# Kernel optimization log

Measured on AMD Instinct MI355X. Metric: run time of the kernel, lower is better.

## Reference

```python
import jax, jax.numpy as jnp
import numpy as np

INF = 1e5
EPS = 1e-8
B, NRES, NRIG = 1, 448, 512
C_S, C_Z, C_H, H, PQ, PV = 384, 128, 16, 12, 4, 8


def _quat_to_rot(q):
    q = q / jnp.linalg.norm(q, axis=-1, keepdims=True)
    w, x, y, z = q[..., 0], q[..., 1], q[..., 2], q[..., 3]
    return jnp.stack([
        jnp.stack([1 - 2 * (y * y + z * z), 2 * (x * y - w * z), 2 * (x * z + w * y)], -1),
        jnp.stack([2 * (x * y + w * z), 1 - 2 * (x * x + z * z), 2 * (y * z - w * x)], -1),
        jnp.stack([2 * (x * z - w * y), 2 * (y * z + w * x), 1 - 2 * (x * x + y * y)], -1),
    ], -2)


def setup_inputs() -> dict:
    key = jax.random.key(0)
    ks = jax.random.split(key, 16)
    lin = lambda k, i, o: (jax.random.normal(k, (i, o), jnp.float32) / np.sqrt(i))
    hc = H * C_H
    return dict(
        s=jax.random.normal(ks[0], (B, NRIG, C_S), jnp.float32),
        z=jax.random.normal(ks[1], (B, NRES, NRES, C_Z), jnp.float32),
        rot=_quat_to_rot(jax.random.normal(ks[2], (B, NRIG, 4), jnp.float32)),
        trans=jax.random.normal(ks[3], (B, NRIG, 3), jnp.float32) * 10.0,
        mask=jnp.ones((B, NRIG), jnp.float32),
        rigid_to_res_idx=jax.random.randint(ks[4], (B, NRIG), 0, NRES),
        w_q=lin(ks[5], C_S, hc), b_q=jnp.zeros((hc,), jnp.float32),
        w_kv=lin(ks[6], C_S, 2 * hc), b_kv=jnp.zeros((2 * hc,), jnp.float32),
        w_qp=lin(ks[7], C_S, H * PQ * 3), b_qp=jnp.zeros((H * PQ * 3,), jnp.float32),
        w_kvp=lin(ks[8], C_S, H * (PQ + PV) * 3), b_kvp=jnp.zeros((H * (PQ + PV) * 3,), jnp.float32),
        w_b=lin(ks[9], C_Z, H), b_b=jnp.zeros((H,), jnp.float32),
        w_dz=lin(ks[10], C_Z, C_Z // 4), b_dz=jnp.zeros((C_Z // 4,), jnp.float32),
        head_weights=jnp.full((H,), 0.5413, jnp.float32),  # softplus^-1(1)
        w_out=lin(ks[11], H * (C_Z // 4 + C_H + PV * 4), C_S),
        b_out=jnp.zeros((C_S,), jnp.float32),
    )


def _fwd(s, z, rot, trans, mask, rigid_to_res_idx,
         w_q, b_q, w_kv, b_kv, w_qp, b_qp, w_kvp, b_kvp,
         w_b, b_b, w_dz, b_dz, head_weights, w_out, b_out):
    Bd, nr, _ = s.shape
    nres = z.shape[-2]
    h = w_b.shape[-1]
    ch = w_q.shape[-1] // h
    pq = w_qp.shape[-1] // (3 * h)
    pkv = w_kvp.shape[-1] // (3 * h)
    pv = pkv - pq

    q = (s @ w_q + b_q).reshape(Bd, nr, h, ch)
    kv = (s @ w_kv + b_kv).reshape(Bd, nr, h, 2 * ch)
    k, v = kv[..., :ch], kv[..., ch:]

    def to_pts(flat):
        # flat: [B,nr,3*D] laid out as 3 coordinate chunks -> global-frame pts [B,nr,D,3]
        D = flat.shape[-1] // 3
        p = jnp.moveaxis(flat.reshape(Bd, nr, 3, D), -2, -1)
        return jnp.einsum('bnij,bndj->bndi', rot, p) + trans[:, :, None, :]

    q_pts = to_pts(s @ w_qp + b_qp).reshape(Bd, nr, h, pq, 3)
    kv_pts = to_pts(s @ w_kvp + b_kvp).reshape(Bd, nr, h, pkv, 3)
    k_pts, v_pts = kv_pts[..., :pq, :], kv_pts[..., pq:, :]

    # pair bias gathered rigid->res on both axes
    bi = jnp.arange(Bd)[:, None, None]
    b_pair = z @ w_b + b_b  # [B,Nres,Nres,H]
    b_bcast = b_pair[bi, rigid_to_res_idx[:, :, None], rigid_to_res_idx[:, None, :]]  # [B,nr,nr,H]

    a = jnp.einsum('bihc,bjhc->bhij', q, k) * np.sqrt(1.0 / (3 * ch))
    a = a + np.sqrt(1.0 / 3) * jnp.moveaxis(b_bcast, -1, -3)

    # squared-distance point attention
    diff = q_pts[:, :, None] - k_pts[:, None]  # [B,nr,nr,h,pq,3]
    sq = jnp.sum(diff * diff, -1)              # [B,nr,nr,h,pq]
    hw = jax.nn.softplus(head_weights) * np.sqrt(1.0 / (3 * (pq * 9.0 / 2)))
    pt_att = -0.5 * jnp.sum(sq * hw[:, None], -1)  # [B,nr,nr,h]
    a = a + jnp.moveaxis(pt_att, -1, -3)

    sq_mask = INF * (mask[:, :, None] * mask[:, None, :] - 1.0)
    a = jax.nn.softmax(a + sq_mask[:, None], axis=-1)  # [B,h,nr,nr]

    o = jnp.einsum('bhij,bjhc->bihc', a, v).reshape(Bd, nr, h * ch)

    o_pt_g = jnp.einsum('bhij,bjhpx->bihpx', a, v_pts)  # [B,nr,h,pv,3]
    o_pt = jnp.einsum('bnji,bnhpj->bnhpi', rot, o_pt_g - trans[:, :, None, None, :])  # invert_apply
    o_pt_norm = jnp.sqrt(jnp.sum(o_pt * o_pt, -1) + EPS).reshape(Bd, nr, h * pv)
    o_pt = o_pt.reshape(Bd, nr, h * pv, 3)

    pair_z = z @ w_dz + b_dz  # [B,Nres,Nres,cz4]
    pz_rig = pair_z[jnp.arange(Bd)[:, None], rigid_to_res_idx]  # [B,nr,Nres,cz4]
    # faithful to the torch scatter_add_: the index varies over the QUERY rigid i
    # (constant over keys j), so row i's full softmax mass lands in column res(i).
    onehot = jax.nn.one_hot(rigid_to_res_idx, nres, dtype=a.dtype)  # [B,nr,Nres]
    a_agg = a.sum(-1)[..., None] * onehot[:, None]  # [B,h,nr,Nres]
    o_pair = jnp.einsum('bhin,bind->bihd', a_agg, pz_rig).reshape(Bd, nr, -1)

    feats = jnp.concatenate([o, o_pt[..., 0], o_pt[..., 1], o_pt[..., 2], o_pt_norm, o_pair], -1)
    return feats @ w_out + b_out


def reference(s, z, rot, trans, mask, rigid_to_res_idx, w_q, b_q, w_kv, b_kv, w_qp, b_qp, w_kvp, b_kvp, w_b, b_b, w_dz, b_dz, head_weights, w_out, b_out):
    return _fwd(s, z, rot, trans, mask, rigid_to_res_idx, w_q, b_q, w_kv, b_kv, w_qp, b_qp, w_kvp, b_kvp, w_b, b_b, w_dz, b_dz, head_weights, w_out, b_out)
```

## Files before the change

### kernel.cpp

```cpp
#include <hip/hip_runtime.h>
#include <hip/hip_bf16.h>
#include <math.h>

constexpr int NRIG = 512;
constexpr int NRES = 448;
constexpr int CS   = 384;
constexpr int CZ   = 128;
constexpr int CH   = 16;
constexpr int NH   = 12;
constexpr int PQ   = 4;
constexpr int PV   = 8;
constexpr int HC   = NH * CH;
constexpr int NPAIR = NRES*NRES;
constexpr float INF_ = 100000.0f;
constexpr float SC_ = 0.57735026918962584f;

constexpr size_t OFF_Q   = 0;
constexpr size_t OFF_KT  = OFF_Q   + (size_t)NH*NRIG*16;
constexpr size_t OFF_QP  = OFF_KT  + (size_t)NH*16*NRIG;
constexpr size_t OFF_KPT = OFF_QP  + (size_t)NH*NRIG*12;
constexpr size_t OFF_VT  = OFF_KPT + (size_t)NH*12*NRIG;
constexpr size_t OFF_O   = OFF_VT  + (size_t)NH*40*NRIG;
constexpr size_t OFF_OPT = OFF_O   + (size_t)NRIG*HC;
constexpr size_t OFF_RS  = OFF_OPT + (size_t)NRIG*NH*PV*3;
constexpr size_t OFF_BP  = OFF_RS  + (size_t)NRIG*NH;
constexpr size_t OFF_RAW = OFF_BP  + (size_t)NH*NPAIR;
constexpr size_t OFF_F   = OFF_RAW + (size_t)NRIG*576;
constexpr size_t OFF_P3  = OFF_F   + (size_t)NRIG*960;

constexpr int ZWB_BLOCKS = NPAIR/64;

__global__ __launch_bounds__(256, 4) void prep_kernel(
    const float* __restrict__ z,  const float* __restrict__ wb, const float* __restrict__ bb,
    const float* __restrict__ s,
    const float* __restrict__ wq,  const float* __restrict__ bq,
    const float* __restrict__ wkv, const float* __restrict__ bkv,
    const float* __restrict__ wqp, const float* __restrict__ bqp,
    const float* __restrict__ wkvp,const float* __restrict__ bkvp,
    float* __restrict__ ws)
{
    __shared__ float smem[3200];
    const int t = threadIdx.x;

    if ((int)blockIdx.x < ZWB_BLOCKS) {
        const int lane = t & 63;
        const int w    = t >> 6;
        const int oct  = lane >> 3;
        const int kl   = lane & 7;
        const int kbase = kl << 4;
        const size_t r0 = (size_t)blockIdx.x * 64;

        float wv[16][3];
        #pragma unroll
        for (int kk = 0; kk < 16; ++kk) {
            #pragma unroll
            for (int j = 0; j < 3; ++j)
                wv[kk][j] = wb[(size_t)(kbase + kk)*12 + 3*w + j];
        }
        const float bb0 = bb[3*w+0], bb1 = bb[3*w+1], bb2 = bb[3*w+2];
        float* bp = ws + OFF_BP + (size_t)(3*w)*NPAIR;

        float4 zbA0, zbA1, zbA2, zbA3;
        float4 zbB0, zbB1, zbB2, zbB3;
        {
            const float4* zp = (const float4*)(z + (r0 + oct)*CZ + kbase);
            zbA0 = zp[0]; zbA1 = zp[1]; zbA2 = zp[2]; zbA3 = zp[3];
        }
        #pragma unroll
        for (int p = 0; p < 8; ++p) {
            if (p < 7) {
                const float4* zp = (const float4*)(z + (r0 + (size_t)(p+1)*8 + oct)*CZ + kbase);
                if ((p & 1) == 0) { zbB0 = zp[0]; zbB1 = zp[1]; zbB2 = zp[2]; zbB3 = zp[3]; }
                else              { zbA0 = zp[0]; zbA1 = zp[1]; zbA2 = zp[2]; zbA3 = zp[3]; }
            }
            const float4 c0 = ((p & 1) == 0) ? zbA0 : zbB0;
            const float4 c1 = ((p & 1) == 0) ? zbA1 : zbB1;
            const float4 c2 = ((p & 1) == 0) ? zbA2 : zbB2;
            const float4 c3 = ((p & 1) == 0) ? zbA3 : zbB3;
            const float zr[16] = {c0.x,c0.y,c0.z,c0.w, c1.x,c1.y,c1.z,c1.w,
                                  c2.x,c2.y,c2.z,c2.w, c3.x,c3.y,c3.z,c3.w};
            float a0 = 0.f, a1 = 0.f, a2 = 0.f;
            #pragma unroll
            for (int kk = 0; kk < 16; ++kk) {
                const float zv = zr[kk];
                a0 += zv*wv[kk][0]; a1 += zv*wv[kk][1]; a2 += zv*wv[kk][2];
            }
            a0 += __shfl_xor(a0,1); a0 += __shfl_xor(a0,2); a0 += __shfl_xor(a0,4);
            a1 += __shfl_xor(a1,1); a1 += __shfl_xor(a1,2); a1 += __shfl_xor(a1,4);
            a2 += __shfl_xor(a2,1); a2 += __shfl_xor(a2,2); a2 += __shfl_xor(a2,4);
            if (kl == 0) {
                const size_t r = r0 + (size_t)p*8 + oct;
                bp[r]                   = (a0 + bb0) * SC_;
                bp[(size_t)NPAIR + r]   = (a1 + bb1) * SC_;
                bp[(size_t)2*NPAIR + r] = (a2 + bb2) * SC_;
            }
        }
    } else {
        constexpr int BM=64, BN=32, BK=32, LDA=68;
        float (*sA)[LDA] = (float(*)[LDA])smem;
        float (*sB)[BN]  = (float(*)[BN])(smem + 2176);
        const int bid = (int)blockIdx.x - ZWB_BLOCKS;
        const int m0 = (bid & 7) * BM;
        const int c0 = (bid >> 3) * BN;
        const int tx = t & 15, ty = t >> 4;

        float acc[4][2] = {};
        for (int kt = 0; kt < CS/BK; ++kt) {
            const int k0 = kt*BK;
            #pragma unroll
            for (int r = 0; r < 2; ++r) {
                int qd = r*256 + t;
                int m = qd >> 3, kq = (qd & 7) << 2;
                float4 f = *(const float4*)(s + (size_t)(m0+m)*CS + k0 + kq);
                sA[kq+0][m] = f.x; sA[kq+1][m] = f.y;
                sA[kq+2][m] = f.z; sA[kq+3][m] = f.w;
            }
            {
                int kk = t >> 3, c4 = (t & 7) << 2;
                int c = c0 + c4;
                const float* wp; int ld, co;
                if (c < 192)      { wp = wq;   ld = 192; co = c;     }
                else if (c < 576) { wp = wkv;  ld = 384; co = c-192; }
                else if (c < 720) { wp = wqp;  ld = 144; co = c-576; }
                else              { wp = wkvp; ld = 432; co = c-720; }
                float4 f = *(const float4*)(wp + (size_t)(k0+kk)*ld + co);
                *(float4*)&sB[kk][c4] = f;
            }
            __syncthreads();
            #pragma unroll
            for (int kk = 0; kk < BK; ++kk) {
                float4 a = *(const float4*)&sA[kk][ty*4];
                float2 b = *(const float2*)&sB[kk][tx*2];
                acc[0][0] += a.x*b.x; acc[0][1] += a.x*b.y;
                acc[1][0] += a.y*b.x; acc[1][1] += a.y*b.y;
                acc[2][0] += a.z*b.x; acc[2][1] += a.z*b.y;
                acc[3][0] += a.w*b.x; acc[3][1] += a.w*b.y;
            }
            __syncthreads();
        }
        float* qw  = ws + OFF_Q;  float* ktw = ws + OFF_KT;  float* vt = ws + OFF_VT;
        float* raw = ws + OFF_RAW;
        #pragma unroll
        for (int i = 0; i < 4; ++i)
            #pragma unroll
            for (int j = 0; j < 2; ++j) {
                int n = m0 + ty*4 + i;
                int c = c0 + tx*2 + j;
                if (c < 192) {
                    int hh = c >> 4, cc = c & 15;
                    qw[((size_t)hh*NRIG + n)*16 + cc] = acc[i][j] + bq[c];
                } else if (c < 576) {
                    int e = c-192; float val = acc[i][j] + bkv[e];
                    int hh = e >> 5, sub = e & 31;
                    if (sub < CH) ktw[((size_t)hh*16 + sub)*NRIG + n] = val;
                    else          vt [((size_t)hh*40 + (sub-CH))*NRIG + n] = val;
                } else {
                    int e = c-576;
                    float bb_ = (c < 720) ? bqp[e] : bkvp[c-720];
                    raw[(size_t)n*576 + e] = acc[i][j] + bb_;
                }
            }
    }
}

__global__ __launch_bounds__(256) void rotate_kernel(
    const float* __restrict__ rot, const float* __restrict__ trans,
    const float* __restrict__ raw_in, float* __restrict__ qpw,
    float* __restrict__ kptw, float* __restrict__ vtw)
{
    const int gid = blockIdx.x*256 + threadIdx.x;
    const int n = gid / 192, d = gid % 192;
    const float* raw = raw_in + (size_t)n*576;
    float px, py, pzz;
    if (d < 48) { px = raw[d];      py = raw[48+d];       pzz = raw[96+d]; }
    else { int dd = d-48; px = raw[144+dd]; py = raw[288+dd]; pzz = raw[432+dd]; }
    const float* R = rot   + (size_t)n*9;
    const float* T = trans + (size_t)n*3;
    float gx = R[0]*px + R[1]*py + R[2]*pzz + T[0];
    float gy = R[3]*px + R[4]*py + R[5]*pzz + T[1];
    float gz = R[6]*px + R[7]*py + R[8]*pzz + T[2];
    if (d < 48) {
        int hh = d >> 2, pp = d & 3;
        float* dst = qpw + ((size_t)hh*NRIG + n)*12 + pp*3;
        dst[0]=gx; dst[1]=gy; dst[2]=gz;
    } else {
        int dd = d-48; int hh = dd/12, pp = dd%12;
        if (pp < PQ) {
            float* kpt = kptw + (size_t)hh*12*NRIG;
            kpt[(size_t)(pp*3+0)*NRIG + n] = gx;
            kpt[(size_t)(pp*3+1)*NRIG + n] = gy;
            kpt[(size_t)(pp*3+2)*NRIG + n] = gz;
        } else {
            float* vt = vtw + ((size_t)hh*40 + 16 + (pp-PQ)*3)*NRIG + n;
            vt[0*NRIG]=gx; vt[1*NRIG]=gy; vt[2*NRIG]=gz;
        }
    }
}

__global__ __launch_bounds__(256) void attn_kernel(
    const float* __restrict__ hw_in, const float* __restrict__ mask,
    const int* __restrict__ ridx,
    const float* __restrict__ qw_all,  const float* __restrict__ ktw_all,
    const float* __restrict__ qpw_all, const float* __restrict__ kpt_all,
    const float* __restrict__ vt_all,  const float* __restrict__ bp_all,
    float* __restrict__ o_out, float* __restrict__ opt_out, float* __restrict__ rs_out)
{
    constexpr int TI = 8;
    const int h    = blockIdx.x;
    const int i0   = blockIdx.y * TI;
    const int t    = threadIdx.x;
    const int lane = t & 63, wid = t >> 6;

    __shared__ float sE[TI*516];
    __shared__ float sP[16][TI][45];
    __shared__ float sS[TI];

    const float* qw  = qw_all  + (size_t)h*NRIG*16;
    const float* ktw = ktw_all + (size_t)h*16*NRIG;
    const float* qpw = qpw_all + (size_t)h*NRIG*12;
    const float* kpt = kpt_all + (size_t)h*12*NRIG;
    const float* vt  = vt_all  + (size_t)h*40*NRIG;
    const float* bph = bp_all  + (size_t)h*NPAIR;

    const float hwv = -0.5f * log1pf(__expf(hw_in[h])) * 0.13608276348795434f;
    const float QKS = 0.14433756729740643f;

    #pragma unroll
    for (int jj = 0; jj < 2; ++jj) {
        const int j = t + jj*256;
        float kk[16], kpv[12];
        #pragma unroll
        for (int c = 0; c < 16; ++c) kk[c]  = ktw[c*NRIG + j];
        #pragma unroll
        for (int e = 0; e < 12; ++e) kpv[e] = kpt[e*NRIG + j];
        const float mj = mask[j];
        const int   rj = ridx[j];
        #pragma unroll
        for (int qq = 0; qq < TI; ++qq) {
            const float* qv  = qw  + (size_t)(i0+qq)*16;
            const float* qpv = qpw + (size_t)(i0+qq)*12;
            const float  mi  = mask[i0+qq];
            const int    ri  = ridx[i0+qq];
            float dot = 0.f;
            #pragma unroll
            for (int c = 0; c < 16; ++c) dot += qv[c]*kk[c];
            float sq = 0.f;
            #pragma unroll
            for (int e = 0; e < 12; ++e) { float d = qpv[e]-kpv[e]; sq += d*d; }
            const float bv = bph[(size_t)ri*NRES + rj];
            const float lgt = dot*QKS + bv + hwv*sq + INF_*(mi*mj - 1.0f);
            sE[qq*516 + j] = __expf(lgt);
        }
    }
    __syncthreads();

    {
        float acc[11][TI];
        #pragma unroll
        for (int ci=0;ci<11;++ci)
            #pragma unroll
            for (int qq=0;qq<TI;++qq) acc[ci][qq]=0.f;

        #pragma unroll
        for (int m = 0; m < 8; ++m) {
            const int j = lane + (m<<6);
            float ev[TI];
            #pragma unroll
            for (int qq=0;qq<TI;++qq) ev[qq] = sE[qq*516 + j];
            #pragma unroll
            for (int ci = 0; ci < 11; ++ci) {
                if (ci < 10 || wid == 0) {
                    const int c = wid + (ci<<2);
                    const float vv = (c == 40) ? 1.0f : vt[(size_t)c*NRIG + j];
                    #pragma unroll
                    for (int qq=0;qq<TI;++qq) acc[ci][qq] += ev[qq]*vv;
                }
            }
        }
        #pragma unroll
        for (int ci=0;ci<11;++ci)
            if (ci < 10 || wid == 0)
                #pragma unroll
                for (int qq=0;qq<TI;++qq) {
                    acc[ci][qq] += __shfl_xor(acc[ci][qq], 1);
                    acc[ci][qq] += __shfl_xor(acc[ci][qq], 2);
                }
        if ((lane & 3) == 0) {
            const int g = lane >> 2;
            #pragma unroll
            for (int ci=0;ci<11;++ci)
                if (ci < 10 || wid == 0) {
                    const int c = wid + (ci<<2);
                    #pragma unroll
                    for (int qq=0;qq<TI;++qq) sP[g][qq][c] = acc[ci][qq];
                }
        }
    }
    __syncthreads();

    if (t < TI) {
        float S = 0.f;
        #pragma unroll
        for (int g = 0; g < 16; ++g) S += sP[g][t][40];
        sS[t] = S;
    }
    __syncthreads();

    for (int e = t; e < TI*41; e += 256) {
        const int qq = e / 41, c = e % 41;
        const int n = i0 + qq;
        float sum = 0.f;
        #pragma unroll
        for (int g = 0; g < 16; ++g) sum += sP[g][qq][c];
        const float val = sum * (1.0f / sS[qq]);
        if (c < 16)       o_out[((size_t)n*NH + h)*CH + c]        = val;
        else if (c < 40)  opt_out[((size_t)n*NH + h)*24 + (c-16)] = val;
        else              rs_out[(size_t)n*NH + h]                = val;
    }
}

__global__ __launch_bounds__(256) void feats_kernel(
    const float* __restrict__ rot, const float* __restrict__ trans,
    const float* __restrict__ z, const int* __restrict__ ridx,
    const float* __restrict__ wdz, const float* __restrict__ bdz,
    const float* __restrict__ o_ws, const float* __restrict__ optg,
    const float* __restrict__ rs, float* __restrict__ F)
{
    constexpr int TI = 4;
    __shared__ float sZd[TI][CZ];
    __shared__ float sPz[TI][32];
    const int i0 = blockIdx.x*TI;
    const int t  = threadIdx.x;

    for (int e = t; e < TI*CZ; e += 256) {
        int qq = e >> 7, c = e & 127;
        int ri = ridx[i0+qq];
        sZd[qq][c] = z[((size_t)ri*NRES + ri)*CZ + c];
    }
    for (int e = t; e < TI*HC; e += 256) {
        int qq = e/HC, c = e%HC;
        F[(size_t)(i0+qq)*960 + c] = o_ws[(size_t)(i0+qq)*HC + c];
    }
    for (int e = t; e < TI*96; e += 256) {
        int qq = e/96, hp = e%96; int n = i0+qq;
        const float* g = optg + ((size_t)n*NH + hp/PV)*24 + (hp%PV)*3;
        float gx = g[0]-trans[n*3+0], gy = g[1]-trans[n*3+1], gz = g[2]-trans[n*3+2];
        const float* R = rot + (size_t)n*9;
        float lx = R[0]*gx + R[3]*gy + R[6]*gz;
        float ly = R[1]*gx + R[4]*gy + R[7]*gz;
        float lz = R[2]*gx + R[5]*gy + R[8]*gz;
        float* Fr = F + (size_t)n*960;
        Fr[192+hp] = lx; Fr[288+hp] = ly; Fr[384+hp] = lz;
        Fr[480+hp] = sqrtf(lx*lx+ly*ly+lz*lz + 1e-8f);
    }
    __syncthreads();
    if (t < TI*32) {
        int qq = t >> 5, d = t & 31;
        float acc = 0.f;
        #pragma unroll 8
        for (int c = 0; c < CZ; ++c) acc += sZd[qq][c] * wdz[(size_t)c*32 + d];
        sPz[qq][d] = acc + bdz[d];
    }
    __syncthreads();
    for (int e = t; e < TI*384; e += 256) {
        int qq = e/384, hd = e%384; int n = i0+qq;
        F[(size_t)n*960 + 576 + hd] = rs[(size_t)n*NH + (hd>>5)] * sPz[qq][hd&31];
    }
}

__global__ __launch_bounds__(256) void out_gemm_kernel(
    const float* __restrict__ w_out, const float* __restrict__ F,
    float* __restrict__ P)
{
    constexpr int BM=64, BN=32, BK=32, LDA=68;
    __shared__ float sA[BK][LDA];
    __shared__ float sB[BK][BN];
    const int m0 = blockIdx.x * BM;
    const int c0 = blockIdx.y * BN;
    const int ks = blockIdx.z;
    const int t  = threadIdx.x;
    const int tx = t & 15, ty = t >> 4;

    float acc[4][2] = {};
    for (int kt = 0; kt < 10; ++kt) {
        const int k0 = ks*320 + kt*BK;
        #pragma unroll
        for (int r = 0; r < 2; ++r) {
            int qd = r*256 + t;
            int m = qd >> 3, kq = (qd & 7) << 2;
            float4 f = *(const float4*)(F + (size_t)(m0+m)*960 + k0 + kq);
            sA[kq+0][m] = f.x; sA[kq+1][m] = f.y;
            sA[kq+2][m] = f.z; sA[kq+3][m] = f.w;
        }
        {
            int kk = t >> 3, c4 = (t & 7) << 2;
            float4 f = *(const float4*)(w_out + (size_t)(k0+kk)*CS + c0 + c4);
            *(float4*)&sB[kk][c4] = f;
        }
        __syncthreads();
        #pragma unroll
        for (int kk = 0; kk < BK; ++kk) {
            float4 a = *(const float4*)&sA[kk][ty*4];
            float2 b = *(const float2*)&sB[kk][tx*2];
            acc[0][0] += a.x*b.x; acc[0][1] += a.x*b.y;
            acc[1][0] += a.y*b.x; acc[1][1] += a.y*b.y;
            acc[2][0] += a.z*b.x; acc[2][1] += a.z*b.y;
            acc[3][0] += a.w*b.x; acc[3][1] += a.w*b.y;
        }
        __syncthreads();
    }
    #pragma unroll
    for (int i = 0; i < 4; ++i)
        #pragma unroll
        for (int j = 0; j < 2; ++j) {
            int n = m0 + ty*4 + i;
            int c = c0 + tx*2 + j;
            P[(size_t)ks*NRIG*CS + (size_t)n*CS + c] = acc[i][j];
        }
}

__global__ __launch_bounds__(256) void reduce_kernel(
    const float* __restrict__ P, const float* __restrict__ b_out,
    float* __restrict__ out)
{
    const int i4 = blockIdx.x*256 + threadIdx.x;
    const size_t base = (size_t)i4 * 4;
    float4 a = *(const float4*)(P + base);
    float4 b = *(const float4*)(P + (size_t)NRIG*CS + base);
    float4 c = *(const float4*)(P + (size_t)2*NRIG*CS + base);
    const int cc = (int)(base % CS);
    float4 bv = *(const float4*)(b_out + cc);
    float4 r;
    r.x = a.x+b.x+c.x+bv.x; r.y = a.y+b.y+c.y+bv.y;
    r.z = a.z+b.z+c.z+bv.z; r.w = a.w+b.w+c.w+bv.w;
    *(float4*)(out + base) = r;
}

extern "C" void kernel_launch(void* const* d_in, const int* in_sizes, int n_in,
                              void* d_out, int out_size, void* d_ws, size_t ws_size,
                              hipStream_t stream)
{
    const float* s     = (const float*)d_in[0];
    const float* z     = (const float*)d_in[1];
    const float* rot   = (const float*)d_in[2];
    const float* trans = (const float*)d_in[3];
    const float* mask  = (const float*)d_in[4];
    const int*   ridx  = (const int*)  d_in[5];
    const float* wq    = (const float*)d_in[6];
    const float* bq    = (const float*)d_in[7];
    const float* wkv   = (const float*)d_in[8];
    const float* bkv   = (const float*)d_in[9];
    const float* wqp   = (const float*)d_in[10];
    const float* bqp   = (const float*)d_in[11];
    const float* wkvp  = (const float*)d_in[12];
    const float* bkvp  = (const float*)d_in[13];
    const float* wb    = (const float*)d_in[14];
    const float* bb    = (const float*)d_in[15];
    const float* wdz   = (const float*)d_in[16];
    const float* bdz   = (const float*)d_in[17];
    const float* hw    = (const float*)d_in[18];
    const float* wout  = (const float*)d_in[19];
    const float* bout  = (const float*)d_in[20];
    float* ws  = (float*)d_ws;
    float* out = (float*)d_out;

    hipLaunchKernelGGL(prep_kernel, dim3(ZWB_BLOCKS + 288), dim3(256), 0, stream,
        z, wb, bb, s, wq,bq, wkv,bkv, wqp,bqp, wkvp,bkvp, ws);
    hipLaunchKernelGGL(rotate_kernel, dim3(NRIG*192/256), dim3(256), 0, stream,
        rot, trans, ws+OFF_RAW, ws+OFF_QP, ws+OFF_KPT, ws+OFF_VT);
    hipLaunchKernelGGL(attn_kernel, dim3(NH, NRIG/8), dim3(256), 0, stream,
        hw, mask, ridx, ws+OFF_Q, ws+OFF_KT, ws+OFF_QP, ws+OFF_KPT,
        ws+OFF_VT, ws+OFF_BP, ws+OFF_O, ws+OFF_OPT, ws+OFF_RS);
    hipLaunchKernelGGL(feats_kernel, dim3(NRIG/4), dim3(256), 0, stream,
        rot, trans, z, ridx, wdz, bdz, ws+OFF_O, ws+OFF_OPT, ws+OFF_RS, ws+OFF_F);
    hipLaunchKernelGGL(out_gemm_kernel, dim3(NRIG/64, CS/32, 3), dim3(256), 0, stream,
        wout, ws+OFF_F, ws+OFF_P3);
    hipLaunchKernelGGL(reduce_kernel, dim3(NRIG*CS/4/256), dim3(256), 0, stream,
        ws+OFF_P3, bout, out);
}
```

Baseline: 130.2 us.

## Process 256 pair rows per z-bias block with a simple rolled load loop

```diff
diff --git a/kernel.cpp b/kernel.cpp
--- a/kernel.cpp
+++ b/kernel.cpp
@@ -28,9 +28,9 @@
 constexpr size_t OFF_F   = OFF_RAW + (size_t)NRIG*576;
 constexpr size_t OFF_P3  = OFF_F   + (size_t)NRIG*960;
 
-constexpr int ZWB_BLOCKS = NPAIR/64;
-
-__global__ __launch_bounds__(256, 4) void prep_kernel(
+constexpr int ZWB_BLOCKS = NPAIR/256;
+
+__global__ __launch_bounds__(256, 2) void prep_kernel(
     const float* __restrict__ z,  const float* __restrict__ wb, const float* __restrict__ bb,
     const float* __restrict__ s,
     const float* __restrict__ wq,  const float* __restrict__ bq,
@@ -48,51 +48,36 @@
         const int oct  = lane >> 3;
         const int kl   = lane & 7;
         const int kbase = kl << 4;
-        const size_t r0 = (size_t)blockIdx.x * 64;
-
-        float wv[16][3];
+        const size_t r0 = (size_t)blockIdx.x * 256;
+
+        float w0[16], w1[16], w2[16];
         #pragma unroll
         for (int kk = 0; kk < 16; ++kk) {
-            #pragma unroll
-            for (int j = 0; j < 3; ++j)
-                wv[kk][j] = wb[(size_t)(kbase + kk)*12 + 3*w + j];
+            const float* wp = wb + (size_t)(kbase + kk)*12 + 3*w;
+            w0[kk] = wp[0]; w1[kk] = wp[1]; w2[kk] = wp[2];
         }
         const float bb0 = bb[3*w+0], bb1 = bb[3*w+1], bb2 = bb[3*w+2];
         float* bp = ws + OFF_BP + (size_t)(3*w)*NPAIR;
 
-        float4 zbA0, zbA1, zbA2, zbA3;
-        float4 zbB0, zbB1, zbB2, zbB3;
-        {
-            const float4* zp = (const float4*)(z + (r0 + oct)*CZ + kbase);
-            zbA0 = zp[0]; zbA1 = zp[1]; zbA2 = zp[2]; zbA3 = zp[3];
-        }
-        #pragma unroll
-        for (int p = 0; p < 8; ++p) {
-            if (p < 7) {
-                const float4* zp = (const float4*)(z + (r0 + (size_t)(p+1)*8 + oct)*CZ + kbase);
-                if ((p & 1) == 0) { zbB0 = zp[0]; zbB1 = zp[1]; zbB2 = zp[2]; zbB3 = zp[3]; }
-                else              { zbA0 = zp[0]; zbA1 = zp[1]; zbA2 = zp[2]; zbA3 = zp[3]; }
-            }
-            const float4 c0 = ((p & 1) == 0) ? zbA0 : zbB0;
-            const float4 c1 = ((p & 1) == 0) ? zbA1 : zbB1;
-            const float4 c2 = ((p & 1) == 0) ? zbA2 : zbB2;
-            const float4 c3 = ((p & 1) == 0) ? zbA3 : zbB3;
+        for (int p = 0; p < 32; ++p) {
+            const size_t row = r0 + (size_t)p*8 + oct;
+            const float4* zp = (const float4*)(z + row*CZ + kbase);
+            const float4 c0 = zp[0], c1 = zp[1], c2 = zp[2], c3 = zp[3];
             const float zr[16] = {c0.x,c0.y,c0.z,c0.w, c1.x,c1.y,c1.z,c1.w,
                                   c2.x,c2.y,c2.z,c2.w, c3.x,c3.y,c3.z,c3.w};
             float a0 = 0.f, a1 = 0.f, a2 = 0.f;
             #pragma unroll
             for (int kk = 0; kk < 16; ++kk) {
                 const float zv = zr[kk];
-                a0 += zv*wv[kk][0]; a1 += zv*wv[kk][1]; a2 += zv*wv[kk][2];
+                a0 += zv*w0[kk]; a1 += zv*w1[kk]; a2 += zv*w2[kk];
             }
             a0 += __shfl_xor(a0,1); a0 += __shfl_xor(a0,2); a0 += __shfl_xor(a0,4);
             a1 += __shfl_xor(a1,1); a1 += __shfl_xor(a1,2); a1 += __shfl_xor(a1,4);
             a2 += __shfl_xor(a2,1); a2 += __shfl_xor(a2,2); a2 += __shfl_xor(a2,4);
             if (kl == 0) {
-                const size_t r = r0 + (size_t)p*8 + oct;
-                bp[r]                   = (a0 + bb0) * SC_;
-                bp[(size_t)NPAIR + r]   = (a1 + bb1) * SC_;
-                bp[(size_t)2*NPAIR + r] = (a2 + bb2) * SC_;
+                bp[row]                   = (a0 + bb0) * SC_;
+                bp[(size_t)NPAIR + row]   = (a1 + bb1) * SC_;
+                bp[(size_t)2*NPAIR + row] = (a2 + bb2) * SC_;
             }
         }
     } else {
```

Result: faster. 106.3 us (-18.4%).
